# Kernel tuning notes

Measured on AMD Instinct MI355X. Metric: run time of the kernel, lower is better.

## Reference

```python
import jax, jax.numpy as jnp
import numpy as np

B, C, DET, N_ANGLES = 8, 1, 512, 180


def _ramp_filter_coeffs(size):
    # scikit-image style spatial-domain ramp kernel -> FFT (used by pytorch_radon RampFilter)
    n = np.concatenate([np.arange(1, size // 2 + 1, 2), np.arange(size // 2 - 1, 0, -2)])
    f = np.zeros(size)
    f[0] = 0.25
    f[1::2] = -1.0 / (np.pi * n) ** 2
    return (2.0 * np.real(np.fft.fft(f))).astype(np.float32)


def _ramp_filter(x):
    # x: [B, C, D, A]; filter along detector dim D
    D = x.shape[2]
    padded = max(64, int(2 ** np.ceil(np.log2(2 * D))))
    xp = jnp.pad(x, ((0, 0), (0, 0), (0, padded - D), (0, 0)))
    filt = jnp.asarray(_ramp_filter_coeffs(padded))[:, None]  # [padded, 1] broadcasts over angles
    proj = jnp.fft.fft(xp, axis=2) * filt
    return jnp.real(jnp.fft.ifft(proj, axis=2))[:, :, :D, :]


def setup_inputs() -> dict:
    key = jax.random.key(0)
    x = jax.random.normal(key, (B, C, DET, N_ANGLES), dtype=jnp.float32)
    return {"x": x}


def reference(x):
    b, c, D, A = x.shape
    S = D  # circle=True -> in_size == it_size
    xs = _ramp_filter(x)

    theta = jnp.arange(A, dtype=jnp.float32) * (jnp.pi / 180.0)  # deg2rad(arange(180))
    u = jnp.linspace(-1.0, 1.0, S, dtype=jnp.float32)
    ygrid = u[:, None]  # varies along rows (meshgrid 'ij' first output)
    xgrid = u[None, :]  # varies along cols

    cols = jnp.moveaxis(xs, 3, 0)  # [A, B, C, D] one filtered projection per angle

    def body(reco, inp):
        col, th = inp  # col: [B, C, D]
        # grid_sample with align_corners=True: X picks column i_theta exactly;
        # Y = x*cos(th) - y*sin(th) is the normalized detector coordinate.
        t = xgrid * jnp.cos(th) - ygrid * jnp.sin(th)          # [S, S]
        yi = (t + 1.0) * 0.5 * (D - 1)                          # unnormalize (align_corners=True)
        i0 = jnp.floor(yi).astype(jnp.int32)
        w = yi - i0.astype(jnp.float32)
        i1 = i0 + 1
        v0 = jnp.where((i0 >= 0) & (i0 < D), col[:, :, jnp.clip(i0, 0, D - 1)], 0.0)
        v1 = jnp.where((i1 >= 0) & (i1 < D), col[:, :, jnp.clip(i1, 0, D - 1)], 0.0)
        return reco + v0 * (1.0 - w) + v1 * w, None

    reco0 = jnp.zeros((b, c, S, S), dtype=jnp.float32)
    reco, _ = jax.lax.scan(body, reco0, (cols, theta))

    circle = (xgrid ** 2 + ygrid ** 2) <= 1.0  # [S, S]
    reco = jnp.where(circle, reco, 0.0)
    return reco * (jnp.pi / (2.0 * A))
```

## Files before the change

kernel.cpp:

```cpp
#include <hip/hip_runtime.h>
#include <hip/hip_fp16.h>
#include <math.h>

#define DET 512
#define NA 180
#define NTILES 1024
#define TANG_FLOATS (NTILES * NA * 4)
#define CHUNK 5
#define WWIN 24
#define NCH 18
#define NSLOT (CHUNK * WWIN * 2)
#define NBUF 4
#define ZERO_IDX (NA * DET * 2)
#define PREPB 360

typedef _Float16 half2_t __attribute__((ext_vector_type(2)));

__device__ __forceinline__ void async_copy16(void* lds, const void* g) {
    __builtin_amdgcn_global_load_lds(
        (const __attribute__((address_space(1))) unsigned*)g,
        (__attribute__((address_space(3))) unsigned*)(unsigned)(unsigned long long)lds,
        16, 0, 0);
}


__global__ __launch_bounds__(512) void prep_filter_kernel(const float* __restrict__ x,
                                                          float4* __restrict__ tang,
                                                          unsigned* __restrict__ xsT2,
                                                          float4* __restrict__ out4) {
    const int t = threadIdx.x;
    if (blockIdx.x >= 4 * NA) {
        const int pb = blockIdx.x - 4 * NA;
        int idx = pb * 512 + t;
        if (idx < NTILES * NA) {
            int tile = idx / NA;
            int a = idx - tile * NA;
            float th = (float)a * 0.017453292519943295f;
            float C = 255.5f * cosf(th);
            float S = 255.5f * sinf(th);
            int x0 = (tile & 31) << 4, y0 = (tile >> 5) << 4;
            float xga = (float)(2 * x0 - 511)        * (1.0f / 511.0f);
            float xgb = (float)(2 * (x0 + 15) - 511) * (1.0f / 511.0f);
            float yga = (float)(2 * y0 - 511)        * (1.0f / 511.0f);
            float ygb = (float)(2 * (y0 + 15) - 511) * (1.0f / 511.0f);
            float mn = 255.5f + fminf(xga * C, xgb * C) + fminf(-yga * S, -ygb * S);
            int w0 = (int)floorf(mn) - 1;
            tang[idx] = make_float4(255.5f - (float)w0, C, S, __int_as_float(w0));
        }
        if (pb == 0 && t == 0) {
            uint4* z = (uint4*)xsT2 + ZERO_IDX;
            *z = make_uint4(0u, 0u, 0u, 0u);
        }
        for (int q = t; q < 1457; q += 512) {
            int o = pb * 1457 + q;
            if (o < (1 << 19))
                out4[o] = make_float4(0.0f, 0.0f, 0.0f, 0.0f);
        }
        return;
    }

    __shared__ float xcols[2][DET];
    __shared__ __align__(16) float god_raw[520];
    __shared__ float part[8][DET];
    float* godp = god_raw + 4;

    const int a = blockIdx.x >> 2;
    const int z = blockIdx.x & 3;

    for (int i = t; i < 520; i += 512) {
        int m = i - 4;
        float g = 0.0f;
        if (m >= 0) {
            float fk = (float)(2 * m + 1 - 512);
            g = -0.20264236728467558f / (fk * fk);
        }
        god_raw[i] = g;
    }
    for (int i = t; i < 2 * DET; i += 512) {
        int b = i >> 9, j = i & 511;
        xcols[b][j] = x[((2 * z + b) * DET + j) * NA + a];
    }
    __syncthreads();

    const int w  = t >> 6, l = t & 63;
    const int lb = w >> 2, q = w & 3;
    const int d0 = l << 3;
    const int jstart = q << 7;

    float acc[8];
#pragma unroll
    for (int r = 0; r < 8; ++r) acc[r] = 0.0f;

    int b = 252 + (d0 >> 1) - (q << 6);
    float Wod[12];
    *(float4*)(Wod)     = *(const float4*)(godp + b - 4);
    *(float4*)(Wod + 4) = *(const float4*)(godp + b);
    *(float4*)(Wod + 8) = *(const float4*)(godp + b + 4);
    float xv[8];
    *(float4*)(xv)     = *(const float4*)(&xcols[lb][jstart]);
    *(float4*)(xv + 4) = *(const float4*)(&xcols[lb][jstart + 4]);

    for (int j0 = jstart; j0 < jstart + 128; j0 += 8) {
        float nxv[8]; float4 nw;
        const bool more = (j0 < jstart + 120);
        if (more) {
            *(float4*)(nxv)     = *(const float4*)(&xcols[lb][j0 + 8]);
            *(float4*)(nxv + 4) = *(const float4*)(&xcols[lb][j0 + 12]);
            nw = *(const float4*)(godp + b - 8);
        }
#pragma unroll
        for (int jj = 0; jj < 8; ++jj)
#pragma unroll
            for (int r = ((jj + 1) & 1); r < 8; r += 2)
                acc[r] = fmaf(xv[jj], Wod[4 + ((7 + r - jj) >> 1)], acc[r]);
        if (more) {
#pragma unroll
            for (int i = 7; i >= 0; --i) Wod[i + 4] = Wod[i];
            *(float4*)(Wod) = nw;
#pragma unroll
            for (int i = 0; i < 8; ++i) xv[i] = nxv[i];
            b -= 4;
        }
    }

    if ((d0 >> 7) == q) {
        float xd[8];
        *(float4*)(xd)     = *(const float4*)(&xcols[lb][d0]);
        *(float4*)(xd + 4) = *(const float4*)(&xcols[lb][d0 + 4]);
#pragma unroll
        for (int r = 0; r < 8; ++r) acc[r] = fmaf(0.5f, xd[r], acc[r]);
    }

    *(float4*)(&part[w][d0])     = *(const float4*)(acc);
    *(float4*)(&part[w][d0 + 4]) = *(const float4*)(acc + 4);
    __syncthreads();

    for (int i = t; i < DET; i += 512) {
        unsigned pw[2];
#pragma unroll
        for (int bq = 0; bq < 2; ++bq) {
            float v0 = (part[4 * bq][i]     + part[4 * bq + 1][i])
                     + (part[4 * bq + 2][i] + part[4 * bq + 3][i]);
            float v1 = 0.0f;
            if (i < DET - 1)
                v1 = (part[4 * bq][i + 1]     + part[4 * bq + 1][i + 1])
                   + (part[4 * bq + 2][i + 1] + part[4 * bq + 3][i + 1]);
            __half2 hh = __halves2half2(__float2half_rn(v0), __float2half_rn(v1 - v0));
            pw[bq] = *(unsigned*)&hh;
        }
        *(uint2*)(xsT2 + ((size_t)a * DET + i) * 8 + 4 * (z >> 1) + 2 * (z & 1)) =
            make_uint2(pw[0], pw[1]);
    }
}

__global__ __launch_bounds__(256, 8) void backproj_kernel(const float4* __restrict__ tang,
                                                          const uint4* __restrict__ xs,
                                                          float* __restrict__ out) {
    __shared__ uint4 win[NBUF][NSLOT];
    __shared__ int   wtab[90];

    const int tile = blockIdx.x & 1023;
    const int abase = (blockIdx.x >> 10) * 90;
    const int x0 = (tile & 31) << 4, y0 = (tile >> 5) << 4;
    const int t = threadIdx.x;
    const int px = t & 15, py = t >> 4;
    const float xg = (float)(2 * (x0 + px) - 511) * (1.0f / 511.0f);
    const float yg = (float)(2 * (y0 + py) - 511) * (1.0f / 511.0f);

    float acc[8];
#pragma unroll
    for (int j = 0; j < 8; ++j) acc[j] = 0.0f;

    const float4* ta = tang + (size_t)tile * NA;
    const uint4*  zs = xs + ZERO_IDX;

    const int gg_pre  = (t >= CHUNK * WWIN) ? 1 : 0;
    const int r_pre   = t - gg_pre * (CHUNK * WWIN);
    const int ci_pre  = r_pre / WWIN;
    const int off_pre = r_pre - ci_pre * WWIN;

    if (t < 90) wtab[t] = __float_as_int(ta[abase + t].w);
    __syncthreads();

#define STAGE(CC)                                                              \
    {                                                                          \
        int cc = (CC);                                                         \
        if (t < NSLOT) {                                                       \
            int a = cc * CHUNK + ci_pre;                                       \
            int d = wtab[a] + off_pre;                                         \
            const uint4* src = ((unsigned)d < 512u)                            \
                ? &xs[((size_t)(abase + a) * DET + d) * 2 + gg_pre] : zs;      \
            async_copy16(&win[cc & 3][t & 192], src);                          \
        }                                                                      \
    }

    STAGE(0); STAGE(1); STAGE(2);

    for (int c = 0; c < NCH; ++c) {
        if (c < NCH - 2)       asm volatile("s_waitcnt vmcnt(2)" ::: "memory");
        else if (c == NCH - 2) asm volatile("s_waitcnt vmcnt(1)" ::: "memory");
        else                   asm volatile("s_waitcnt vmcnt(0)" ::: "memory");
        __builtin_amdgcn_s_barrier();
        __builtin_amdgcn_sched_barrier(0);

        if (c + 3 < NCH) STAGE(c + 3);

        const uint4* base = &win[c & 3][0];
#pragma unroll
        for (int ci = 0; ci < CHUNK; ++ci) {
            float4 A = ta[abase + c * CHUNK + ci];
            float yv = fmaf(xg, A.y, A.x) - yg * A.z;
            float fi = floorf(yv);
            int  off = (int)fi;
            float wgt = yv - fi;
            auto pkw = __builtin_amdgcn_cvt_pkrtz(1.0f, wgt);
            half2_t wv = *(half2_t*)&pkw;
            uint4 u0 = base[ci * WWIN + off];
            uint4 u1 = base[CHUNK * WWIN + ci * WWIN + off];
            acc[0] = __builtin_amdgcn_fdot2(*(half2_t*)&u0.x, wv, acc[0], false);
            acc[1] = __builtin_amdgcn_fdot2(*(half2_t*)&u0.y, wv, acc[1], false);
            acc[2] = __builtin_amdgcn_fdot2(*(half2_t*)&u0.z, wv, acc[2], false);
            acc[3] = __builtin_amdgcn_fdot2(*(half2_t*)&u0.w, wv, acc[3], false);
            acc[4] = __builtin_amdgcn_fdot2(*(half2_t*)&u1.x, wv, acc[4], false);
            acc[5] = __builtin_amdgcn_fdot2(*(half2_t*)&u1.y, wv, acc[5], false);
            acc[6] = __builtin_amdgcn_fdot2(*(half2_t*)&u1.z, wv, acc[6], false);
            acc[7] = __builtin_amdgcn_fdot2(*(half2_t*)&u1.w, wv, acc[7], false);
        }
    }

    const float r2 = xg * xg + yg * yg;
    const float m  = (r2 <= 1.0f) ? 0.008726646259971648f : 0.0f;
    const size_t pbase = ((size_t)(y0 + py) << 9) + (size_t)(x0 + px);
#pragma unroll
    for (int j = 0; j < 8; ++j)
        atomicAdd(&out[((size_t)j << 18) + pbase], acc[j] * m);
}

extern "C" void kernel_launch(void* const* d_in, const int* in_sizes, int n_in,
                              void* d_out, int out_size, void* d_ws, size_t ws_size,
                              hipStream_t stream) {
    const float* x = (const float*)d_in[0];
    float* out = (float*)d_out;
    float* ws  = (float*)d_ws;

    float4*   tang = (float4*)ws;
    unsigned* xsT2 = (unsigned*)(ws + TANG_FLOATS);

    prep_filter_kernel<<<4 * NA + PREPB, 512, 0, stream>>>(x, tang, xsT2, (float4*)out);
    backproj_kernel<<<2 * NTILES, 256, 0, stream>>>(tang, (const uint4*)xsT2, out);
}
```

Before: 97.61 us.

## Merge angle halves into one block and reduce in LDS instead of atomics

Each backprojection block now holds 512 threads, and its two halves cover the two 90-angle ranges of the same tile, each with its own LDS window buffers. The halves combine their partial sums through shared memory, and the result goes to the output with plain stores rather than atomicAdd. Because of this, the prep kernel no longer has to zero the 16MB output. The cost is a larger per-block LDS footprint and an extra barrier-based reduction, which may lower occupancy.

```diff
diff --git a/kernel.cpp b/kernel.cpp
--- a/kernel.cpp
+++ b/kernel.cpp
@@ -26,8 +26,7 @@
 
 __global__ __launch_bounds__(512) void prep_filter_kernel(const float* __restrict__ x,
                                                           float4* __restrict__ tang,
-                                                          unsigned* __restrict__ xsT2,
-                                                          float4* __restrict__ out4) {
+                                                          unsigned* __restrict__ xsT2) {
     const int t = threadIdx.x;
     if (blockIdx.x >= 4 * NA) {
         const int pb = blockIdx.x - 4 * NA;
@@ -51,11 +50,6 @@
             uint4* z = (uint4*)xsT2 + ZERO_IDX;
             *z = make_uint4(0u, 0u, 0u, 0u);
         }
-        for (int q = t; q < 1457; q += 512) {
-            int o = pb * 1457 + q;
-            if (o < (1 << 19))
-                out4[o] = make_float4(0.0f, 0.0f, 0.0f, 0.0f);
-        }
         return;
     }
 
@@ -153,17 +147,19 @@
     }
 }
 
-__global__ __launch_bounds__(256, 8) void backproj_kernel(const float4* __restrict__ tang,
+__global__ __launch_bounds__(512, 4) void backproj_kernel(const float4* __restrict__ tang,
                                                           const uint4* __restrict__ xs,
                                                           float* __restrict__ out) {
-    __shared__ uint4 win[NBUF][NSLOT];
-    __shared__ int   wtab[90];
-
-    const int tile = blockIdx.x & 1023;
-    const int abase = (blockIdx.x >> 10) * 90;
+    __shared__ uint4 win[2][NBUF][NSLOT];
+    __shared__ int   wtab[NA];
+
+    const int tile = blockIdx.x;
     const int x0 = (tile & 31) << 4, y0 = (tile >> 5) << 4;
     const int t = threadIdx.x;
-    const int px = t & 15, py = t >> 4;
+    const int hh = t >> 8;
+    const int tl = t & 255;
+    const int abase = hh * 90;
+    const int px = tl & 15, py = tl >> 4;
     const float xg = (float)(2 * (x0 + px) - 511) * (1.0f / 511.0f);
     const float yg = (float)(2 * (y0 + py) - 511) * (1.0f / 511.0f);
 
@@ -174,23 +170,23 @@
     const float4* ta = tang + (size_t)tile * NA;
     const uint4*  zs = xs + ZERO_IDX;
 
-    const int gg_pre  = (t >= CHUNK * WWIN) ? 1 : 0;
-    const int r_pre   = t - gg_pre * (CHUNK * WWIN);
+    const int gg_pre  = (tl >= CHUNK * WWIN) ? 1 : 0;
+    const int r_pre   = tl - gg_pre * (CHUNK * WWIN);
     const int ci_pre  = r_pre / WWIN;
     const int off_pre = r_pre - ci_pre * WWIN;
 
-    if (t < 90) wtab[t] = __float_as_int(ta[abase + t].w);
+    if (t < NA) wtab[t] = __float_as_int(ta[t].w);
     __syncthreads();
 
 #define STAGE(CC)                                                              \
     {                                                                          \
         int cc = (CC);                                                         \
-        if (t < NSLOT) {                                                       \
+        if (tl < NSLOT) {                                                      \
             int a = cc * CHUNK + ci_pre;                                       \
-            int d = wtab[a] + off_pre;                                         \
+            int d = wtab[abase + a] + off_pre;                                 \
             const uint4* src = ((unsigned)d < 512u)                            \
                 ? &xs[((size_t)(abase + a) * DET + d) * 2 + gg_pre] : zs;      \
-            async_copy16(&win[cc & 3][t & 192], src);                          \
+            async_copy16(&win[hh][cc & 3][tl & 192], src);                     \
         }                                                                      \
     }
 
@@ -205,7 +201,7 @@
 
         if (c + 3 < NCH) STAGE(c + 3);
 
-        const uint4* base = &win[c & 3][0];
+        const uint4* base = &win[hh][c & 3][0];
 #pragma unroll
         for (int ci = 0; ci < CHUNK; ++ci) {
             float4 A = ta[abase + c * CHUNK + ci];
@@ -228,12 +224,21 @@
         }
     }
 
-    const float r2 = xg * xg + yg * yg;
-    const float m  = (r2 <= 1.0f) ? 0.008726646259971648f : 0.0f;
-    const size_t pbase = ((size_t)(y0 + py) << 9) + (size_t)(x0 + px);
-#pragma unroll
-    for (int j = 0; j < 8; ++j)
-        atomicAdd(&out[((size_t)j << 18) + pbase], acc[j] * m);
+    __syncthreads();
+    float* red = (float*)&win[0][0][0];
+    if (hh == 1) {
+#pragma unroll
+        for (int j = 0; j < 8; ++j) red[j * 256 + tl] = acc[j];
+    }
+    __syncthreads();
+    if (hh == 0) {
+        const float r2 = xg * xg + yg * yg;
+        const float m  = (r2 <= 1.0f) ? 0.008726646259971648f : 0.0f;
+        const size_t pbase = ((size_t)(y0 + py) << 9) + (size_t)(x0 + px);
+#pragma unroll
+        for (int j = 0; j < 8; ++j)
+            out[((size_t)j << 18) + pbase] = (acc[j] + red[j * 256 + tl]) * m;
+    }
 }
 
 extern "C" void kernel_launch(void* const* d_in, const int* in_sizes, int n_in,
@@ -246,6 +251,6 @@
     float4*   tang = (float4*)ws;
     unsigned* xsT2 = (unsigned*)(ws + TANG_FLOATS);
 
-    prep_filter_kernel<<<4 * NA + PREPB, 512, 0, stream>>>(x, tang, xsT2, (float4*)out);
-    backproj_kernel<<<2 * NTILES, 256, 0, stream>>>(tang, (const uint4*)xsT2, out);
-}
+    prep_filter_kernel<<<4 * NA + PREPB, 512, 0, stream>>>(x, tang, xsT2);
+    backproj_kernel<<<NTILES, 512, 0, stream>>>(tang, (const uint4*)xsT2, out);
+}
```

New measurement: 101.9 us. 1.04x slower.
